# Kernel tuning notes

Measured on AMD Instinct MI355X. Metric: run time of the kernel, lower is better.

Reference implementation:

```python
import jax, jax.numpy as jnp
import numpy as np

MUL = 128          # multiplicity of every irrep block
A0 = float(np.sqrt(0.5))   # component norm: dim(0e)=1 / (2 paths into out0)
A1 = float(np.sqrt(1.5))   # dim(1o)=3 / (2 paths into out1)
A2 = float(np.sqrt(3.0))   # dim(1e)=3 / (1 path into out2)


def _cg():
    """Real Clebsch-Gordan (wigner-3j, e3nn convention) tensors for l<=1 paths."""
    eye = np.eye(3)
    eps = np.zeros((3, 3, 3))
    eps[0, 1, 2] = eps[1, 2, 0] = eps[2, 0, 1] = 1.0
    eps[0, 2, 1] = eps[2, 1, 0] = eps[1, 0, 2] = -1.0
    C000 = np.ones((1, 1, 1))
    C011 = eye.reshape(1, 3, 3) / np.sqrt(3.0)
    C101 = eye.reshape(3, 1, 3) / np.sqrt(3.0)
    C110 = eye.reshape(3, 3, 1) / np.sqrt(3.0)
    C111 = eps / np.sqrt(6.0)
    return [jnp.asarray(c, jnp.float32) for c in (C000, C011, C101, C110, C111)]


def setup_inputs() -> dict:
    key = jax.random.key(0)
    k1, k2, k3 = jax.random.split(key, 3)
    N = 100000
    x1 = jax.random.normal(k1, (N, 4 * MUL), dtype=jnp.float32)   # 128x0e + 128x1o
    x2 = jax.random.normal(k2, (N, 4), dtype=jnp.float32)          # 1x0e + 1x1o
    weight = jax.random.normal(k3, (5 * MUL,), dtype=jnp.float32)  # 5 uvu paths x (128,1)
    return {"x1": x1, "x2": x2, "weight": weight}


def _tp(xa, xb, C, wp, alpha):
    # uvu path with mul2 broadcast: out[n,u,k] = alpha * w[u] * sum_{v,i,j} xa[n,u,i] xb[n,v,j] C[i,j,k]
    return (alpha * wp)[None, :, None] * jnp.einsum('nui,nvj,ijk->nuk', xa, xb, C)


def reference(x1, x2, weight):
    N = x1.shape[0]
    x1_0 = x1[:, :MUL].reshape(N, MUL, 1)        # 128x0e
    x1_1 = x1[:, MUL:].reshape(N, MUL, 3)        # 128x1o
    x2_0 = x2[:, :1].reshape(N, 1, 1)            # 1x0e
    x2_1 = x2[:, 1:].reshape(N, 1, 3)            # 1x1o
    w = weight.reshape(5, MUL)                    # per-instruction (mul1, mul2=1) blocks
    C000, C011, C101, C110, C111 = _cg()

    out0 = _tp(x1_0, x2_0, C000, w[0], A0) + _tp(x1_1, x2_1, C110, w[3], A0)  # -> 128x0e
    out1 = _tp(x1_0, x2_1, C011, w[1], A1) + _tp(x1_1, x2_0, C101, w[2], A1)  # -> 128x1o
    out2 = _tp(x1_1, x2_1, C111, w[4], A2)                                     # -> 128x1e

    return jnp.concatenate(
        [out0.reshape(N, MUL), out1.reshape(N, 3 * MUL), out2.reshape(N, 3 * MUL)],
        axis=-1,
    )
```

## Files before the change

kernel.cpp:

```cpp
#include <hip/hip_runtime.h>

#define MUL   128
#define ROWS  8
#define BLOCK 256

__global__ __launch_bounds__(BLOCK) void tp_kernel(
    const float* __restrict__ x1, const float* __restrict__ x2,
    const float* __restrict__ w, float* __restrict__ out, int N)
{
    const float S  = 0.70710678118654752440f;
    const float S6 = 0.40824829046386301637f;

    __shared__ float buf[ROWS * 896];

    int n0   = blockIdx.x * ROWS;
    int rows = N - n0; if (rows > ROWS) rows = ROWS;
    int tid  = threadIdx.x;

    {
        const float4* src = reinterpret_cast<const float4*>(x1 + (size_t)n0 * (4 * MUL));
        float4*       dst = reinterpret_cast<float4*>(buf);
        int nf4 = rows * 128;
#pragma unroll
        for (int k = 0; k < 4; ++k) {
            int g = tid + k * BLOCK;
            if (g < nf4) dst[g] = src[g];
        }
    }
    __syncthreads();

    int r = tid >> 5;
    int t = tid & 31;
    bool active = (r < rows);

    float o0[4], o1[12], o2[12];
    if (active) {
        const float* xr = buf + r * 512;
        float4 a0 = *reinterpret_cast<const float4*>(xr + 4 * t);
        const float4* a1p = reinterpret_cast<const float4*>(xr + MUL + 12 * t);
        float4 p = a1p[0], q = a1p[1], rr = a1p[2];
        float4 b = *reinterpret_cast<const float4*>(x2 + (size_t)(n0 + r) * 4);
        float4 w0 = *reinterpret_cast<const float4*>(w + 0 * MUL + 4 * t);
        float4 w1 = *reinterpret_cast<const float4*>(w + 1 * MUL + 4 * t);
        float4 w2 = *reinterpret_cast<const float4*>(w + 2 * MUL + 4 * t);
        float4 w3 = *reinterpret_cast<const float4*>(w + 3 * MUL + 4 * t);
        float4 w4 = *reinterpret_cast<const float4*>(w + 4 * MUL + 4 * t);

        float a0u[4] = {a0.x, a0.y, a0.z, a0.w};
        float ax[4]  = {p.x, p.w, q.z, rr.y};
        float ay[4]  = {p.y, q.x, q.w, rr.z};
        float az[4]  = {p.z, q.y, rr.x, rr.w};
        float w0u[4] = {w0.x, w0.y, w0.z, w0.w};
        float w1u[4] = {w1.x, w1.y, w1.z, w1.w};
        float w2u[4] = {w2.x, w2.y, w2.z, w2.w};
        float w3u[4] = {w3.x, w3.y, w3.z, w3.w};
        float w4u[4] = {w4.x, w4.y, w4.z, w4.w};

#pragma unroll
        for (int u = 0; u < 4; ++u) {
            float dot = ax[u] * b.y + ay[u] * b.z + az[u] * b.w;
            o0[u] = S * w0u[u] * a0u[u] * b.x + S6 * w3u[u] * dot;
            o1[3 * u + 0] = S * (w1u[u] * a0u[u] * b.y + w2u[u] * ax[u] * b.x);
            o1[3 * u + 1] = S * (w1u[u] * a0u[u] * b.z + w2u[u] * ay[u] * b.x);
            o1[3 * u + 2] = S * (w1u[u] * a0u[u] * b.w + w2u[u] * az[u] * b.x);
            float cx = ay[u] * b.w - az[u] * b.z;
            float cy = az[u] * b.y - ax[u] * b.w;
            float cz = ax[u] * b.z - ay[u] * b.y;
            o2[3 * u + 0] = S * w4u[u] * cx;
            o2[3 * u + 1] = S * w4u[u] * cy;
            o2[3 * u + 2] = S * w4u[u] * cz;
        }
    }
    __syncthreads();

    if (active) {
        float* orow = buf + r * 896;
        *reinterpret_cast<float4*>(orow + 4 * t) =
            make_float4(o0[0], o0[1], o0[2], o0[3]);
        float4* o1p = reinterpret_cast<float4*>(orow + MUL + 12 * t);
        o1p[0] = make_float4(o1[0], o1[1], o1[2],  o1[3]);
        o1p[1] = make_float4(o1[4], o1[5], o1[6],  o1[7]);
        o1p[2] = make_float4(o1[8], o1[9], o1[10], o1[11]);
        float4* o2p = reinterpret_cast<float4*>(orow + 4 * MUL + 12 * t);
        o2p[0] = make_float4(o2[0], o2[1], o2[2],  o2[3]);
        o2p[1] = make_float4(o2[4], o2[5], o2[6],  o2[7]);
        o2p[2] = make_float4(o2[8], o2[9], o2[10], o2[11]);
    }
    __syncthreads();

    {
        const float4* srcb = reinterpret_cast<const float4*>(buf);
        float4*       dstg = reinterpret_cast<float4*>(out + (size_t)n0 * 896);
        int nf4 = rows * 224;
#pragma unroll
        for (int k = 0; k < 7; ++k) {
            int g = tid + k * BLOCK;
            if (g < nf4) dstg[g] = srcb[g];
        }
    }
}

extern "C" void kernel_launch(void* const* d_in, const int* in_sizes, int n_in,
                              void* d_out, int out_size, void* d_ws, size_t ws_size,
                              hipStream_t stream) {
    const float* x1 = (const float*)d_in[0];
    const float* x2 = (const float*)d_in[1];
    const float* w  = (const float*)d_in[2];
    float* out      = (float*)d_out;
    int N = in_sizes[0] / (4 * MUL);
    int blocks = (N + ROWS - 1) / ROWS;
    tp_kernel<<<blocks, BLOCK, 0, stream>>>(x1, x2, w, out, N);
}
```

Baseline: 109.9 us.

## Write outputs directly to global with coalesced float4 mapping, stage weights in LDS

Removes the shared-memory staging of the output tile and the two barriers around it. Each thread now computes output elements in a coalesced float4-per-lane layout and writes them straight to global memory, gathering the scalar inputs it needs from LDS with per-element index math (div by 3, selects). Weights and x2 rows are also staged in LDS once per block. This trades the LDS round trip and syncs for extra integer arithmetic and scattered LDS reads.

```diff
diff --git a/kernel.cpp b/kernel.cpp
--- a/kernel.cpp
+++ b/kernel.cpp
@@ -3,6 +3,10 @@
 #define MUL   128
 #define ROWS  8
 #define BLOCK 256
+
+__device__ __forceinline__ float sel3(int k, float v0, float v1, float v2) {
+    return (k == 0) ? v0 : ((k == 1) ? v1 : v2);
+}
 
 __global__ __launch_bounds__(BLOCK) void tp_kernel(
     const float* __restrict__ x1, const float* __restrict__ x2,
@@ -11,15 +15,17 @@
     const float S  = 0.70710678118654752440f;
     const float S6 = 0.40824829046386301637f;
 
-    __shared__ float buf[ROWS * 896];
+    __shared__ float xs[ROWS * 512];
+    __shared__ float ws[5 * MUL];
+    __shared__ float bs[ROWS * 4];
 
     int n0   = blockIdx.x * ROWS;
     int rows = N - n0; if (rows > ROWS) rows = ROWS;
     int tid  = threadIdx.x;
 
     {
-        const float4* src = reinterpret_cast<const float4*>(x1 + (size_t)n0 * (4 * MUL));
-        float4*       dst = reinterpret_cast<float4*>(buf);
+        const float4* src = reinterpret_cast<const float4*>(x1 + (size_t)n0 * 512);
+        float4*       dst = reinterpret_cast<float4*>(xs);
         int nf4 = rows * 128;
 #pragma unroll
         for (int k = 0; k < 4; ++k) {
@@ -27,76 +33,85 @@
             if (g < nf4) dst[g] = src[g];
         }
     }
+    if (tid < 160)
+        reinterpret_cast<float4*>(ws)[tid] = reinterpret_cast<const float4*>(w)[tid];
+    if (tid < rows)
+        reinterpret_cast<float4*>(bs)[tid] =
+            reinterpret_cast<const float4*>(x2 + (size_t)n0 * 4)[tid];
     __syncthreads();
 
     int r = tid >> 5;
     int t = tid & 31;
-    bool active = (r < rows);
+    if (r >= rows) return;
 
-    float o0[4], o1[12], o2[12];
-    if (active) {
-        const float* xr = buf + r * 512;
+    const float* xr = xs + r * 512;
+    const float* ar = xr + 128;
+    float4 b  = *reinterpret_cast<const float4*>(bs + 4 * r);
+    float* outr = out + (size_t)(n0 + r) * 896;
+
+    {
         float4 a0 = *reinterpret_cast<const float4*>(xr + 4 * t);
-        const float4* a1p = reinterpret_cast<const float4*>(xr + MUL + 12 * t);
+        const float4* a1p = reinterpret_cast<const float4*>(ar + 12 * t);
         float4 p = a1p[0], q = a1p[1], rr = a1p[2];
-        float4 b = *reinterpret_cast<const float4*>(x2 + (size_t)(n0 + r) * 4);
-        float4 w0 = *reinterpret_cast<const float4*>(w + 0 * MUL + 4 * t);
-        float4 w1 = *reinterpret_cast<const float4*>(w + 1 * MUL + 4 * t);
-        float4 w2 = *reinterpret_cast<const float4*>(w + 2 * MUL + 4 * t);
-        float4 w3 = *reinterpret_cast<const float4*>(w + 3 * MUL + 4 * t);
-        float4 w4 = *reinterpret_cast<const float4*>(w + 4 * MUL + 4 * t);
-
+        float4 w0 = *reinterpret_cast<const float4*>(ws + 0 * MUL + 4 * t);
+        float4 w3 = *reinterpret_cast<const float4*>(ws + 3 * MUL + 4 * t);
         float a0u[4] = {a0.x, a0.y, a0.z, a0.w};
         float ax[4]  = {p.x, p.w, q.z, rr.y};
         float ay[4]  = {p.y, q.x, q.w, rr.z};
         float az[4]  = {p.z, q.y, rr.x, rr.w};
         float w0u[4] = {w0.x, w0.y, w0.z, w0.w};
-        float w1u[4] = {w1.x, w1.y, w1.z, w1.w};
-        float w2u[4] = {w2.x, w2.y, w2.z, w2.w};
         float w3u[4] = {w3.x, w3.y, w3.z, w3.w};
-        float w4u[4] = {w4.x, w4.y, w4.z, w4.w};
-
+        float o[4];
 #pragma unroll
         for (int u = 0; u < 4; ++u) {
             float dot = ax[u] * b.y + ay[u] * b.z + az[u] * b.w;
-            o0[u] = S * w0u[u] * a0u[u] * b.x + S6 * w3u[u] * dot;
-            o1[3 * u + 0] = S * (w1u[u] * a0u[u] * b.y + w2u[u] * ax[u] * b.x);
-            o1[3 * u + 1] = S * (w1u[u] * a0u[u] * b.z + w2u[u] * ay[u] * b.x);
-            o1[3 * u + 2] = S * (w1u[u] * a0u[u] * b.w + w2u[u] * az[u] * b.x);
-            float cx = ay[u] * b.w - az[u] * b.z;
-            float cy = az[u] * b.y - ax[u] * b.w;
-            float cz = ax[u] * b.z - ay[u] * b.y;
-            o2[3 * u + 0] = S * w4u[u] * cx;
-            o2[3 * u + 1] = S * w4u[u] * cy;
-            o2[3 * u + 2] = S * w4u[u] * cz;
+            o[u] = S * w0u[u] * a0u[u] * b.x + S6 * w3u[u] * dot;
         }
+        reinterpret_cast<float4*>(outr)[t] = make_float4(o[0], o[1], o[2], o[3]);
     }
-    __syncthreads();
 
-    if (active) {
-        float* orow = buf + r * 896;
-        *reinterpret_cast<float4*>(orow + 4 * t) =
-            make_float4(o0[0], o0[1], o0[2], o0[3]);
-        float4* o1p = reinterpret_cast<float4*>(orow + MUL + 12 * t);
-        o1p[0] = make_float4(o1[0], o1[1], o1[2],  o1[3]);
-        o1p[1] = make_float4(o1[4], o1[5], o1[6],  o1[7]);
-        o1p[2] = make_float4(o1[8], o1[9], o1[10], o1[11]);
-        float4* o2p = reinterpret_cast<float4*>(orow + 4 * MUL + 12 * t);
-        o2p[0] = make_float4(o2[0], o2[1], o2[2],  o2[3]);
-        o2p[1] = make_float4(o2[4], o2[5], o2[6],  o2[7]);
-        o2p[2] = make_float4(o2[8], o2[9], o2[10], o2[11]);
+#pragma unroll
+    for (int j = 0; j < 3; ++j) {
+        int m  = t + 32 * j;
+        int e0 = 4 * m;
+        float4 a1v = *reinterpret_cast<const float4*>(ar + e0);
+        float a1e[4] = {a1v.x, a1v.y, a1v.z, a1v.w};
+        float o[4];
+#pragma unroll
+        for (int jj = 0; jj < 4; ++jj) {
+            int e = e0 + jj;
+            int u = e / 3;
+            int k = e - 3 * u;
+            float bk  = sel3(k, b.y, b.z, b.w);
+            float a0u = xr[u];
+            float w1u = ws[1 * MUL + u];
+            float w2u = ws[2 * MUL + u];
+            o[jj] = S * (w1u * a0u * bk + w2u * a1e[jj] * b.x);
+        }
+        reinterpret_cast<float4*>(outr + MUL)[m] = make_float4(o[0], o[1], o[2], o[3]);
     }
-    __syncthreads();
 
-    {
-        const float4* srcb = reinterpret_cast<const float4*>(buf);
-        float4*       dstg = reinterpret_cast<float4*>(out + (size_t)n0 * 896);
-        int nf4 = rows * 224;
 #pragma unroll
-        for (int k = 0; k < 7; ++k) {
-            int g = tid + k * BLOCK;
-            if (g < nf4) dstg[g] = srcb[g];
+    for (int j = 0; j < 3; ++j) {
+        int m  = t + 32 * j;
+        int e0 = 4 * m;
+        float o[4];
+#pragma unroll
+        for (int jj = 0; jj < 4; ++jj) {
+            int e  = e0 + jj;
+            int u  = e / 3;
+            int k  = e - 3 * u;
+            int k1 = (k == 2) ? 0 : k + 1;
+            int k2 = (k == 0) ? 1 : ((k == 1) ? 2 : 0);
+            k2 = (k == 0) ? 2 : ((k == 1) ? 0 : 1);
+            float s1 = ar[3 * u + k1];
+            float s2 = ar[3 * u + k2];
+            float bk1 = sel3(k1, b.y, b.z, b.w);
+            float bk2 = sel3(k2, b.y, b.z, b.w);
+            float w4u = ws[4 * MUL + u];
+            o[jj] = S * w4u * (s1 * bk2 - s2 * bk1);
         }
+        reinterpret_cast<float4*>(outr + 4 * MUL)[m] = make_float4(o[0], o[1], o[2], o[3]);
     }
 }
 
```

New measurement: 111.5 us. No clear change (+1.5%).
